# Kernel optimization log

Hardware: AMD Instinct MI355X
Metric: run time of the kernel (lower is better)

Reference implementation:

```python
import jax, jax.numpy as jnp
import numpy as np

L, B, D, H, E, K, R = 256, 64, 1024, 16, 8, 2, 64
SCALE_ADAPTER = 0.1


def setup_inputs() -> dict:
    key = jax.random.key(0)
    ks = jax.random.split(key, 10)
    rn = lambda k, shape, s=0.02: jax.random.normal(k, shape, jnp.float32) * s
    return {
        "x": jax.random.normal(ks[0], (L, B, D), jnp.float32),
        "ln1_w": jnp.ones((D,), jnp.float32), "ln1_b": jnp.zeros((D,), jnp.float32),
        "in_proj_w": rn(ks[1], (3 * D, D)), "in_proj_b": jnp.zeros((3 * D,), jnp.float32),
        "out_proj_w": rn(ks[2], (D, D)), "out_proj_b": jnp.zeros((D,), jnp.float32),
        "ln2_w": jnp.ones((D,), jnp.float32), "ln2_b": jnp.zeros((D,), jnp.float32),
        "c_fc_w": rn(ks[3], (4 * D, D)), "c_fc_b": jnp.zeros((4 * D,), jnp.float32),
        "c_proj_w": rn(ks[4], (D, 4 * D)), "c_proj_b": jnp.zeros((D,), jnp.float32),
        "w_gate": rn(ks[5], (D, E), 0.05),
        "down_w": rn(ks[6], (E, R, D)), "down_b": jnp.zeros((E, R), jnp.float32),
        "up_w": rn(ks[7], (E, D, R)), "up_b": jnp.zeros((E, D), jnp.float32),
    }


def _layer_norm(x, w, b, eps=1e-5):
    mu = x.mean(-1, keepdims=True)
    var = ((x - mu) ** 2).mean(-1, keepdims=True)
    return (x - mu) / jnp.sqrt(var + eps) * w + b


def _mha(x, in_w, in_b, out_w, out_b):
    # x: (L,B,D) sequence-first, self-attention q=k=v=x
    hd = D // H
    qkv = x @ in_w.T + in_b                       # (L,B,3D)
    q, k, v = jnp.split(qkv, 3, axis=-1)
    q = q.reshape(L, B, H, hd)
    k = k.reshape(L, B, H, hd)
    v = v.reshape(L, B, H, hd)
    scores = jnp.einsum("lbhd,mbhd->bhlm", q, k) / jnp.sqrt(jnp.float32(hd))
    attn = jax.nn.softmax(scores, axis=-1)
    o = jnp.einsum("bhlm,mbhd->lbhd", attn, v).reshape(L, B, D)
    return o @ out_w.T + out_b


def _cv_squared(t):
    t = t.astype(jnp.float32)
    return t.var(ddof=1) / (t.mean() ** 2 + 1e-10)


def reference(x, ln1_w, ln1_b, in_proj_w, in_proj_b, out_proj_w, out_proj_b,
              ln2_w, ln2_b, c_fc_w, c_fc_b, c_proj_w, c_proj_b,
              w_gate, down_w, down_b, up_w, up_b):
    x = x + _mha(_layer_norm(x, ln1_w, ln1_b), in_proj_w, in_proj_b, out_proj_w, out_proj_b)

    # --- noisy top-k gating (eval path: no noise), routed on token 0 per sequence ---
    logits = x[0] @ w_gate                                    # (B,E)
    top_v, top_i = jax.lax.top_k(logits, min(K + 1, E))
    gk = jax.nn.softmax(top_v[:, :K], axis=1)                 # (B,K)
    gates = jnp.zeros((B, E), jnp.float32).at[jnp.arange(B)[:, None], top_i[:, :K]].set(gk)
    importance = gates.sum(0)
    load = (gates > 0).sum(0)
    moe_loss = (_cv_squared(importance) + _cv_squared(load)) * 0.01

    # --- dense dispatch/combine: y[l,b] = sum_e gates[b,e] * adapter_e(x[l,b]) ---
    h = jax.nn.relu(jnp.einsum("lbd,erd->lber", x, down_w) + down_b)     # (L,B,E,R)
    y = jnp.einsum("lber,edr,be->lbd", h, up_w, gates) + (gates @ up_b)[None]
    y = y * SCALE_ADAPTER

    # --- MLP (QuickGELU) + parallel adapter residual ---
    h2 = _layer_norm(x, ln2_w, ln2_b) @ c_fc_w.T + c_fc_b
    h2 = h2 * jax.nn.sigmoid(1.702 * h2)
    mlp = h2 @ c_proj_w.T + c_proj_b
    x = x + mlp + y
    return x, moe_loss
```

## Files before the change

### kernel.cpp

```cpp
#include <hip/hip_runtime.h>

typedef unsigned short u16;
typedef unsigned int u32;
typedef __bf16 bf16x8 __attribute__((ext_vector_type(8)));
typedef float f32x4 __attribute__((ext_vector_type(4)));

#define MFMA16(a, b, c) __builtin_amdgcn_mfma_f32_16x16x32_bf16(a, b, c, 0, 0, 0)

__device__ __forceinline__ u16 f2bf(float f) {
  u32 u = __builtin_bit_cast(u32, f);
  u32 r = u + 0x7fffu + ((u >> 16) & 1u);
  return (u16)(r >> 16);
}

__device__ __forceinline__ uint4 cvt8(const float4& a, const float4& b) {
  union { u16 h[8]; uint4 q; } u;
  u.h[0] = f2bf(a.x); u.h[1] = f2bf(a.y); u.h[2] = f2bf(a.z); u.h[3] = f2bf(a.w);
  u.h[4] = f2bf(b.x); u.h[5] = f2bf(b.y); u.h[6] = f2bf(b.z); u.h[7] = f2bf(b.w);
  return u.q;
}

__device__ __forceinline__ void gload16(const u16* g, u16* l) {
  __builtin_amdgcn_global_load_lds(
      (const __attribute__((address_space(1))) u32*)g,
      (__attribute__((address_space(3))) u32*)l, 16, 0, 0);
}

template <int MODE, int ASRC>
__global__ __launch_bounds__(256) void gemm_k(
    const void* __restrict__ Av, int lda,
    const u16* __restrict__ W, int ldb,
    const float* __restrict__ bias, const float* __restrict__ aux0,
    float* __restrict__ outF, u16* __restrict__ outB, int N, int K)
{
  __shared__ u16 As[2][128 * 32];
  __shared__ u16 Bs[2][128 * 32];
  const int tid = threadIdx.x;
  const int nxb = gridDim.x >> 7;
  const int gsz = nxb << 5;
  const int g = blockIdx.x / gsz;
  const int rem = blockIdx.x - g * gsz;
  const int m0 = ((g << 5) + (rem & 31)) * 128;
  const int n0 = (rem >> 5) * 128;
  const int w = tid >> 6, lane = tid & 63, lr = lane & 15, quad = lane >> 4;
  const int wm = (w >> 1) * 64, wn = (w & 1) * 64;

  f32x4 acc[4][4];
  #pragma unroll
  for (int i = 0; i < 4; i++)
    #pragma unroll
    for (int j = 0; j < 4; j++)
      #pragma unroll
      for (int r = 0; r < 4; r++) acc[i][j][r] = 0.f;

  const int srow = w * 32 + (lane >> 2);
  const int scol = (lane & 3) * 8;
  const u16* gB0 = W + (long)(n0 + srow) * ldb + scol;
  const u16* gB1 = gB0 + (long)16 * ldb;
  const int lo = w * 1024;

  const u16* gA0 = nullptr; const u16* gA1 = nullptr;
  const float* F1 = nullptr; const float* F2 = nullptr;
  const int r0 = tid >> 2, ch0 = (tid & 3) * 8;
  if constexpr (ASRC == 0) {
    gA0 = (const u16*)Av + (long)(m0 + srow) * lda + scol;
    gA1 = gA0 + (long)16 * lda;
  } else {
    F1 = (const float*)Av + (long)(m0 + r0) * lda + ch0;
    F2 = (const float*)Av + (long)(m0 + r0 + 64) * lda + ch0;
  }

  int cur = 0;

  if constexpr (ASRC == 0) {
    gload16(gA0, &As[0][lo]);
    gload16(gA1, &As[0][lo + 512]);
    gload16(gB0, &Bs[0][lo]);
    gload16(gB1, &Bs[0][lo + 512]);
  } else {
    float4 p0 = *(const float4*)(F1);
    float4 p1 = *(const float4*)(F1 + 4);
    float4 q0 = *(const float4*)(F2);
    float4 q1 = *(const float4*)(F2 + 4);
    gload16(gB0, &Bs[0][lo]);
    gload16(gB1, &Bs[0][lo + 512]);
    *(uint4*)&As[0][r0 * 32 + ch0] = cvt8(p0, p1);
    *(uint4*)&As[0][(r0 + 64) * 32 + ch0] = cvt8(q0, q1);
  }
  __syncthreads();

  for (int k0 = 0; k0 < K; k0 += 32) {
    const int kn = k0 + 32;
    const bool more = kn < K;

    float4 p0, p1, q0, q1;
    if constexpr (ASRC == 0) {
      if (more) {
        gload16(gA0 + kn, &As[cur ^ 1][lo]);
        gload16(gA1 + kn, &As[cur ^ 1][lo + 512]);
        gload16(gB0 + kn, &Bs[cur ^ 1][lo]);
        gload16(gB1 + kn, &Bs[cur ^ 1][lo + 512]);
      }
    } else {
      if (more) {
        p0 = *(const float4*)(F1 + kn);
        p1 = *(const float4*)(F1 + kn + 4);
        q0 = *(const float4*)(F2 + kn);
        q1 = *(const float4*)(F2 + kn + 4);
        gload16(gB0 + kn, &Bs[cur ^ 1][lo]);
        gload16(gB1 + kn, &Bs[cur ^ 1][lo + 512]);
      }
    }

    const u16* Asc = As[cur];
    const u16* Bsc = Bs[cur];
    bf16x8 bfr[4];
    #pragma unroll
    for (int j = 0; j < 4; j++)
      bfr[j] = *(const bf16x8*)&Bsc[(wn + j * 16 + lr) * 32 + quad * 8];
    #pragma unroll
    for (int i = 0; i < 4; i++) {
      bf16x8 af = *(const bf16x8*)&Asc[(wm + i * 16 + lr) * 32 + quad * 8];
      #pragma unroll
      for (int j = 0; j < 4; j++)
        acc[i][j] = MFMA16(af, bfr[j], acc[i][j]);
    }

    if constexpr (ASRC == 2) {
      if (more) {
        *(uint4*)&As[cur ^ 1][r0 * 32 + ch0] = cvt8(p0, p1);
        *(uint4*)&As[cur ^ 1][(r0 + 64) * 32 + ch0] = cvt8(q0, q1);
      }
    }

    __syncthreads();
    cur ^= 1;
  }

  #pragma unroll
  for (int i = 0; i < 4; i++) {
    #pragma unroll
    for (int j = 0; j < 4; j++) {
      #pragma unroll
      for (int r = 0; r < 4; r++) {
        const int gm = m0 + wm + i * 16 + quad * 4 + r;
        const int gn = n0 + wn + j * 16 + lr;
        const long oidx = (long)gm * N + gn;
        float v = acc[i][j][r];
        if constexpr (MODE == 0) {
          v += bias[gn];
          outB[oidx] = f2bf(v);
        } else if constexpr (MODE == 1) {
          v += bias[gn] + aux0[oidx];
          outF[oidx] = v;
        } else if constexpr (MODE == 2) {
          v += bias[gn];
          v = fmaxf(v, 0.f);
          float g2 = aux0[(gm & 63) * 8 + (gn >> 6)];
          outB[oidx] = f2bf(v * g2);
        } else if constexpr (MODE == 3) {
          outF[oidx] += 0.1f * (v + aux0[(gm & 63) * 1024 + gn]);
        } else if constexpr (MODE == 4) {
          v += bias[gn];
          float e = __expf(-1.702f * v);
          v = v * __builtin_amdgcn_rcpf(1.f + e);
          outB[oidx] = f2bf(v);
        } else {
          if (bias) v += bias[gn];
          outF[oidx] += v;
        }
      }
    }
  }
}

__global__ __launch_bounds__(256) void attn_k(u16* __restrict__ qkv)
{
  __shared__ u16 Vt[64 * 264];
  __shared__ u16 Ps[32 * 264];
  __shared__ float rowstat[64];
  float* red = (float*)Ps;
  const int bh = blockIdx.x, b = bh >> 4, h = bh & 15;
  const int tid = threadIdx.x, w = tid >> 6, lane = tid & 63;
  const int lr = lane & 15, quad = lane >> 4;
  const long base = (long)b * 3072 + h * 64;

  for (int c = tid; c < 2048; c += 256) {
    int m = c >> 3, ch = (c & 7) * 8;
    uint4 vv = *(const uint4*)(qkv + (long)m * 196608 + base + 2048 + ch);
    const u16* s = (const u16*)&vv;
    #pragma unroll
    for (int t = 0; t < 8; t++) Vt[(ch + t) * 264 + m] = s[t];
  }
  __syncthreads();

  for (int qb = 0; qb < 4; qb++) {
    f32x4 acc[4][4];
    #pragma unroll
    for (int i = 0; i < 4; i++)
      #pragma unroll
      for (int j = 0; j < 4; j++)
        #pragma unroll
        for (int r = 0; r < 4; r++) acc[i][j][r] = 0.f;

    #pragma unroll
    for (int ks = 0; ks < 2; ks++) {
      bf16x8 bfr[4];
      #pragma unroll
      for (int j = 0; j < 4; j++) {
        int key = w * 64 + j * 16 + lr;
        bfr[j] = *(const bf16x8*)(qkv + (long)key * 196608 + base + 1024 + ks * 32 + quad * 8);
      }
      #pragma unroll
      for (int i = 0; i < 4; i++) {
        int gq = qb * 64 + i * 16 + lr;
        bf16x8 af = *(const bf16x8*)(qkv + (long)gq * 196608 + base + ks * 32 + quad * 8);
        #pragma unroll
        for (int j = 0; j < 4; j++)
          acc[i][j] = MFMA16(af, bfr[j], acc[i][j]);
      }
    }

    #pragma unroll
    for (int i = 0; i < 4; i++) {
      #pragma unroll
      for (int r = 0; r < 4; r++) {
        float m = -1e30f;
        #pragma unroll
        for (int j = 0; j < 4; j++) {
          float s = acc[i][j][r] * 0.125f;
          acc[i][j][r] = s;
          m = fmaxf(m, s);
        }
        #pragma unroll
        for (int off = 1; off < 16; off <<= 1) m = fmaxf(m, __shfl_xor(m, off));
        if (lr == 0) red[w * 64 + i * 16 + quad * 4 + r] = m;
      }
    }
    __syncthreads();
    if (tid < 64)
      rowstat[tid] = fmaxf(fmaxf(red[tid], red[64 + tid]),
                           fmaxf(red[128 + tid], red[192 + tid]));
    __syncthreads();

    #pragma unroll
    for (int i = 0; i < 4; i++) {
      #pragma unroll
      for (int r = 0; r < 4; r++) {
        float rm = rowstat[i * 16 + quad * 4 + r];
        float s = 0.f;
        #pragma unroll
        for (int j = 0; j < 4; j++) {
          float e = __expf(acc[i][j][r] - rm);
          acc[i][j][r] = e;
          s += e;
        }
        #pragma unroll
        for (int off = 1; off < 16; off <<= 1) s += __shfl_xor(s, off);
        if (lr == 0) red[w * 64 + i * 16 + quad * 4 + r] = s;
      }
    }
    __syncthreads();
    if (tid < 64)
      rowstat[tid] = red[tid] + red[64 + tid] + red[128 + tid] + red[192 + tid];
    __syncthreads();

    #pragma unroll
    for (int hf = 0; hf < 2; hf++) {
      #pragma unroll
      for (int ii = 0; ii < 2; ii++) {
        int i = hf * 2 + ii;
        #pragma unroll
        for (int r = 0; r < 4; r++) {
          int row = i * 16 + quad * 4 + r;
          float inv = 1.f / rowstat[row];
          #pragma unroll
          for (int j = 0; j < 4; j++)
            Ps[(row - hf * 32) * 264 + w * 64 + j * 16 + lr] =
                f2bf(acc[i][j][r] * inv);
        }
      }
      __syncthreads();
      f32x4 o[2];
      #pragma unroll
      for (int j2 = 0; j2 < 2; j2++)
        #pragma unroll
        for (int r = 0; r < 4; r++) o[j2][r] = 0.f;
      #pragma unroll
      for (int ks = 0; ks < 8; ks++) {
        bf16x8 af = *(const bf16x8*)&Ps[((w >> 1) * 16 + lr) * 264 + ks * 32 + quad * 8];
        #pragma unroll
        for (int j2 = 0; j2 < 2; j2++) {
          int j = (w & 1) * 2 + j2;
          bf16x8 bv = *(const bf16x8*)&Vt[(j * 16 + lr) * 264 + ks * 32 + quad * 8];
          o[j2] = MFMA16(af, bv, o[j2]);
        }
      }
      int l0 = qb * 64 + hf * 32 + (w >> 1) * 16 + quad * 4;
      #pragma unroll
      for (int j2 = 0; j2 < 2; j2++) {
        int j = (w & 1) * 2 + j2;
        #pragma unroll
        for (int r = 0; r < 4; r++)
          qkv[(long)(l0 + r) * 196608 + base + j * 16 + lr] = f2bf(o[j2][r]);
      }
      __syncthreads();
    }
  }
}

__global__ __launch_bounds__(256) void ln_k(const float* __restrict__ x,
                                            const float* __restrict__ wt,
                                            const float* __restrict__ bs,
                                            u16* __restrict__ out)
{
  const int tok = blockIdx.x * 4 + (threadIdx.x >> 6);
  const int lane = threadIdx.x & 63;
  const float* xp = x + (long)tok * 1024;
  float4 v[4];
  float s = 0.f, s2 = 0.f;
  #pragma unroll
  for (int t = 0; t < 4; t++) {
    v[t] = *(const float4*)(xp + t * 256 + lane * 4);
    s += v[t].x + v[t].y + v[t].z + v[t].w;
    s2 += v[t].x * v[t].x + v[t].y * v[t].y + v[t].z * v[t].z + v[t].w * v[t].w;
  }
  #pragma unroll
  for (int off = 32; off >= 1; off >>= 1) {
    s += __shfl_xor(s, off);
    s2 += __shfl_xor(s2, off);
  }
  const float m = s * (1.f / 1024.f);
  const float rstd = rsqrtf(s2 * (1.f / 1024.f) - m * m + 1e-5f);
  u16* op = out + (long)tok * 1024;
  #pragma unroll
  for (int t = 0; t < 4; t++) {
    int d = t * 256 + lane * 4;
    float4 wv = *(const float4*)(wt + d);
    float4 bv = *(const float4*)(bs + d);
    union { u16 h[4]; uint2 q; } o;
    o.h[0] = f2bf((v[t].x - m) * rstd * wv.x + bv.x);
    o.h[1] = f2bf((v[t].y - m) * rstd * wv.y + bv.y);
    o.h[2] = f2bf((v[t].z - m) * rstd * wv.z + bv.z);
    o.h[3] = f2bf((v[t].w - m) * rstd * wv.w + bv.w);
    *(uint2*)(op + d) = o.q;
  }
}

__global__ void cvtk(const float* __restrict__ src, u16* __restrict__ dst, int n4)
{
  int i = blockIdx.x * 256 + threadIdx.x;
  if (i >= n4) return;
  float4 v = ((const float4*)src)[i];
  union { u16 h[4]; uint2 q; } o;
  o.h[0] = f2bf(v.x); o.h[1] = f2bf(v.y); o.h[2] = f2bf(v.z); o.h[3] = f2bf(v.w);
  ((uint2*)dst)[i] = o.q;
}

__global__ void wupk(const float* __restrict__ up_w, u16* __restrict__ dst)
{
  int i = blockIdx.x * 256 + threadIdx.x;
  int r = i & 63, e = (i >> 6) & 7, d = i >> 9;
  dst[i] = f2bf(up_w[(e * 1024 + d) * 64 + r]);
}

__global__ __launch_bounds__(256) void gate_k(const float* __restrict__ x1,
                                              const float* __restrict__ wg,
                                              float* __restrict__ gates)
{
  const int wv = threadIdx.x >> 6, lane = threadIdx.x & 63;
  const int b = blockIdx.x * 4 + wv;
  const float* xp = x1 + (long)b * 1024;
  float lg[8];
  #pragma unroll
  for (int e = 0; e < 8; e++) lg[e] = 0.f;
  for (int i = 0; i < 16; i++) {
    int d = i * 64 + lane;
    float xv = xp[d];
    #pragma unroll
    for (int e = 0; e < 8; e++) lg[e] += xv * wg[d * 8 + e];
  }
  #pragma unroll
  for (int e = 0; e < 8; e++)
    #pragma unroll
    for (int off = 32; off >= 1; off >>= 1) lg[e] += __shfl_xor(lg[e], off);
  if (lane == 0) {
    int e1 = 0; float v1 = lg[0];
    #pragma unroll
    for (int e = 1; e < 8; e++) if (lg[e] > v1) { v1 = lg[e]; e1 = e; }
    int e2 = -1; float v2 = -1e30f;
    #pragma unroll
    for (int e = 0; e < 8; e++) if (e != e1 && lg[e] > v2) { v2 = lg[e]; e2 = e; }
    float ex = __expf(v2 - v1);
    float inv = 1.f / (1.f + ex);
    #pragma unroll
    for (int e = 0; e < 8; e++)
      gates[b * 8 + e] = (e == e1) ? inv : ((e == e2) ? ex * inv : 0.f);
  }
}

__global__ void moe_loss_k(const float* __restrict__ gates, float* __restrict__ out)
{
  if (threadIdx.x != 0) return;
  float imp[8], ld[8];
  for (int e = 0; e < 8; e++) { imp[e] = 0.f; ld[e] = 0.f; }
  for (int b = 0; b < 64; b++)
    for (int e = 0; e < 8; e++) {
      float g = gates[b * 8 + e];
      imp[e] += g;
      if (g > 0.f) ld[e] += 1.f;
    }
  float mi = 0.f, ml = 0.f;
  for (int e = 0; e < 8; e++) { mi += imp[e]; ml += ld[e]; }
  mi *= 0.125f; ml *= 0.125f;
  float vi = 0.f, vl = 0.f;
  for (int e = 0; e < 8; e++) {
    float a = imp[e] - mi; vi += a * a;
    float c = ld[e] - ml; vl += c * c;
  }
  vi *= (1.f / 7.f); vl *= (1.f / 7.f);
  out[0] = 0.01f * (vi / (mi * mi + 1e-10f) + vl / (ml * ml + 1e-10f));
}

__global__ __launch_bounds__(256) void gb_k(const float* __restrict__ gates,
                                            const float* __restrict__ up_b,
                                            float* __restrict__ gb)
{
  int b = blockIdx.x, d0 = threadIdx.x * 4;
  float g[8];
  #pragma unroll
  for (int e = 0; e < 8; e++) g[e] = gates[b * 8 + e];
  float s0 = 0, s1 = 0, s2 = 0, s3 = 0;
  #pragma unroll
  for (int e = 0; e < 8; e++) {
    float4 u = *(const float4*)(up_b + e * 1024 + d0);
    s0 += g[e] * u.x; s1 += g[e] * u.y; s2 += g[e] * u.z; s3 += g[e] * u.w;
  }
  float4 r; r.x = s0; r.y = s1; r.z = s2; r.w = s3;
  *(float4*)(gb + b * 1024 + d0) = r;
}

extern "C" void kernel_launch(void* const* d_in, const int* in_sizes, int n_in,
                              void* d_out, int out_size, void* d_ws, size_t ws_size,
                              hipStream_t stream)
{
  (void)in_sizes; (void)n_in; (void)out_size;
  const float* x      = (const float*)d_in[0];
  const float* ln1_w  = (const float*)d_in[1];
  const float* ln1_b  = (const float*)d_in[2];
  const float* in_w   = (const float*)d_in[3];
  const float* in_b   = (const float*)d_in[4];
  const float* out_w  = (const float*)d_in[5];
  const float* out_b  = (const float*)d_in[6];
  const float* ln2_w  = (const float*)d_in[7];
  const float* ln2_b  = (const float*)d_in[8];
  const float* fc_w   = (const float*)d_in[9];
  const float* fc_b   = (const float*)d_in[10];
  const float* pj_w   = (const float*)d_in[11];
  const float* pj_b   = (const float*)d_in[12];
  const float* w_gate = (const float*)d_in[13];
  const float* down_w = (const float*)d_in[14];
  const float* down_b = (const float*)d_in[15];
  const float* up_w   = (const float*)d_in[16];
  const float* up_b   = (const float*)d_in[17];
  float* out = (float*)d_out;
  char* ws = (char*)d_ws;

  u16* wb_in   = (u16*)(ws + 0);
  u16* wb_out  = (u16*)(ws + 6291456);
  u16* wb_down = (u16*)(ws + 8388608);
  u16* wb_up   = (u16*)(ws + 9437184);
  u16* wb_fc   = (u16*)(ws + 0);
  u16* wb_pj   = (u16*)(ws + 10485760);
  float* gates = (float*)(ws + 19005440);
  float* gb    = (float*)(ws + 19007488);
  u16* qkv     = (u16*)(ws + 19269632);
  u16* xln2    = (u16*)(ws + 19269632);
  u16* hg      = (u16*)(ws + 52824064);
  u16* h2      = (u16*)(ws + 69601280);
  u16* xln = (u16*)d_out;

  const bool big = ws_size >= (size_t)203819008;

  cvtk<<<3072, 256, 0, stream>>>(in_w, wb_in, 786432);
  cvtk<<<1024, 256, 0, stream>>>(out_w, wb_out, 262144);
  cvtk<<<512, 256, 0, stream>>>(down_w, wb_down, 131072);
  wupk<<<2048, 256, 0, stream>>>(up_w, wb_up);

  ln_k<<<4096, 256, 0, stream>>>(x, ln1_w, ln1_b, xln);
  gemm_k<0, 0><<<24 * 128, 256, 0, stream>>>(
      xln, 1024, wb_in, 1024, in_b, nullptr, nullptr, qkv, 3072, 1024);

  attn_k<<<1024, 256, 0, stream>>>(qkv);

  gemm_k<1, 0><<<8 * 128, 256, 0, stream>>>(
      qkv, 3072, wb_out, 1024, out_b, x, out, nullptr, 1024, 1024);

  gate_k<<<16, 256, 0, stream>>>(out, w_gate, gates);
  moe_loss_k<<<1, 64, 0, stream>>>(gates, out + 16777216);
  gb_k<<<64, 256, 0, stream>>>(gates, up_b, gb);

  ln_k<<<4096, 256, 0, stream>>>(out, ln2_w, ln2_b, xln2);

  gemm_k<2, 2><<<4 * 128, 256, 0, stream>>>(
      out, 1024, wb_down, 1024, down_b, gates, nullptr, hg, 512, 1024);
  gemm_k<3, 0><<<8 * 128, 256, 0, stream>>>(
      hg, 512, wb_up, 512, nullptr, gb, out, nullptr, 1024, 512);

  cvtk<<<4096, 256, 0, stream>>>(fc_w, wb_fc, 1048576);
  cvtk<<<4096, 256, 0, stream>>>(pj_w, wb_pj, 1048576);

  if (big) {
    gemm_k<4, 0><<<32 * 128, 256, 0, stream>>>(
        xln2, 1024, wb_fc, 1024, fc_b, nullptr, nullptr, h2, 4096, 1024);
    gemm_k<5, 0><<<8 * 128, 256, 0, stream>>>(
        h2, 4096, wb_pj, 4096, pj_b, nullptr, out, nullptr, 1024, 4096);
  } else {
    for (int c = 0; c < 4; c++) {
      gemm_k<4, 0><<<8 * 128, 256, 0, stream>>>(
          xln2, 1024, wb_fc + (long)c * 1048576, 1024, fc_b + c * 1024,
          nullptr, nullptr, h2, 1024, 1024);
      gemm_k<5, 0><<<8 * 128, 256, 0, stream>>>(
          h2, 1024, wb_pj + c * 1024, 4096, (c == 0) ? pj_b : nullptr,
          nullptr, out, nullptr, 1024, 1024);
    }
  }
}
```

Measured before the change: 1.053 ms.

## Deepen GEMM async LDS pipeline to four stages with vmcnt waits

For bf16-input GEMMs the shared-memory ring grows from two to four buffers. Three tiles are prefetched with direct global-to-LDS loads, and explicit s_waitcnt vmcnt counts replace the full sync, so only one barrier per k-step remains. The goal is to hide global memory latency better. In exchange it uses twice the LDS, which may lower occupancy, and the hand-written waitcnt assumes every thread issues exactly four loads per stage.

```diff
diff --git a/kernel.cpp b/kernel.cpp
--- a/kernel.cpp
+++ b/kernel.cpp
@@ -33,8 +33,9 @@
     const float* __restrict__ bias, const float* __restrict__ aux0,
     float* __restrict__ outF, u16* __restrict__ outB, int N, int K)
 {
-  __shared__ u16 As[2][128 * 32];
-  __shared__ u16 Bs[2][128 * 32];
+  constexpr int NBUF = (ASRC == 0) ? 4 : 2;
+  __shared__ u16 As[NBUF][128 * 32];
+  __shared__ u16 Bs[NBUF][128 * 32];
   const int tid = threadIdx.x;
   const int nxb = gridDim.x >> 7;
   const int gsz = nxb << 5;
@@ -70,38 +71,65 @@
     F2 = (const float*)Av + (long)(m0 + r0 + 64) * lda + ch0;
   }
 
-  int cur = 0;
+  auto compute_tile = [&](const u16* Asc, const u16* Bsc) {
+    bf16x8 bfr[4];
+    #pragma unroll
+    for (int j = 0; j < 4; j++)
+      bfr[j] = *(const bf16x8*)&Bsc[(wn + j * 16 + lr) * 32 + quad * 8];
+    #pragma unroll
+    for (int i = 0; i < 4; i++) {
+      bf16x8 af = *(const bf16x8*)&Asc[(wm + i * 16 + lr) * 32 + quad * 8];
+      #pragma unroll
+      for (int j = 0; j < 4; j++)
+        acc[i][j] = MFMA16(af, bfr[j], acc[i][j]);
+    }
+  };
 
   if constexpr (ASRC == 0) {
-    gload16(gA0, &As[0][lo]);
-    gload16(gA1, &As[0][lo + 512]);
-    gload16(gB0, &Bs[0][lo]);
-    gload16(gB1, &Bs[0][lo + 512]);
+    const int nt = K >> 5;
+    #pragma unroll
+    for (int p = 0; p < 3; p++) {
+      const int kk = p * 32;
+      gload16(gA0 + kk, &As[p][lo]);
+      gload16(gA1 + kk, &As[p][lo + 512]);
+      gload16(gB0 + kk, &Bs[p][lo]);
+      gload16(gB1 + kk, &Bs[p][lo + 512]);
+    }
+    for (int t = 0; t < nt; t++) {
+      if (t < nt - 2)      asm volatile("s_waitcnt vmcnt(8)" ::: "memory");
+      else if (t < nt - 1) asm volatile("s_waitcnt vmcnt(4)" ::: "memory");
+      else                 asm volatile("s_waitcnt vmcnt(0)" ::: "memory");
+      __builtin_amdgcn_s_barrier();
+      asm volatile("" ::: "memory");
+      const int tp = t + 3;
+      if (tp < nt) {
+        const int kn = tp * 32;
+        u16* a = As[tp & 3];
+        u16* b = Bs[tp & 3];
+        gload16(gA0 + kn, a + lo);
+        gload16(gA1 + kn, a + lo + 512);
+        gload16(gB0 + kn, b + lo);
+        gload16(gB1 + kn, b + lo + 512);
+      }
+      compute_tile(As[t & 3], Bs[t & 3]);
+    }
   } else {
-    float4 p0 = *(const float4*)(F1);
-    float4 p1 = *(const float4*)(F1 + 4);
-    float4 q0 = *(const float4*)(F2);
-    float4 q1 = *(const float4*)(F2 + 4);
-    gload16(gB0, &Bs[0][lo]);
-    gload16(gB1, &Bs[0][lo + 512]);
-    *(uint4*)&As[0][r0 * 32 + ch0] = cvt8(p0, p1);
-    *(uint4*)&As[0][(r0 + 64) * 32 + ch0] = cvt8(q0, q1);
-  }
-  __syncthreads();
-
-  for (int k0 = 0; k0 < K; k0 += 32) {
-    const int kn = k0 + 32;
-    const bool more = kn < K;
-
-    float4 p0, p1, q0, q1;
-    if constexpr (ASRC == 0) {
-      if (more) {
-        gload16(gA0 + kn, &As[cur ^ 1][lo]);
-        gload16(gA1 + kn, &As[cur ^ 1][lo + 512]);
-        gload16(gB0 + kn, &Bs[cur ^ 1][lo]);
-        gload16(gB1 + kn, &Bs[cur ^ 1][lo + 512]);
-      }
-    } else {
+    int cur = 0;
+    {
+      float4 p0 = *(const float4*)(F1);
+      float4 p1 = *(const float4*)(F1 + 4);
+      float4 q0 = *(const float4*)(F2);
+      float4 q1 = *(const float4*)(F2 + 4);
+      gload16(gB0, &Bs[0][lo]);
+      gload16(gB1, &Bs[0][lo + 512]);
+      *(uint4*)&As[0][r0 * 32 + ch0] = cvt8(p0, p1);
+      *(uint4*)&As[0][(r0 + 64) * 32 + ch0] = cvt8(q0, q1);
+    }
+    __syncthreads();
+    for (int k0 = 0; k0 < K; k0 += 32) {
+      const int kn = k0 + 32;
+      const bool more = kn < K;
+      float4 p0, p1, q0, q1;
       if (more) {
         p0 = *(const float4*)(F1 + kn);
         p1 = *(const float4*)(F1 + kn + 4);
@@ -110,31 +138,14 @@
         gload16(gB0 + kn, &Bs[cur ^ 1][lo]);
         gload16(gB1 + kn, &Bs[cur ^ 1][lo + 512]);
       }
-    }
-
-    const u16* Asc = As[cur];
-    const u16* Bsc = Bs[cur];
-    bf16x8 bfr[4];
-    #pragma unroll
-    for (int j = 0; j < 4; j++)
-      bfr[j] = *(const bf16x8*)&Bsc[(wn + j * 16 + lr) * 32 + quad * 8];
-    #pragma unroll
-    for (int i = 0; i < 4; i++) {
-      bf16x8 af = *(const bf16x8*)&Asc[(wm + i * 16 + lr) * 32 + quad * 8];
-      #pragma unroll
-      for (int j = 0; j < 4; j++)
-        acc[i][j] = MFMA16(af, bfr[j], acc[i][j]);
-    }
-
-    if constexpr (ASRC == 2) {
+      compute_tile(As[cur], Bs[cur]);
       if (more) {
         *(uint4*)&As[cur ^ 1][r0 * 32 + ch0] = cvt8(p0, p1);
         *(uint4*)&As[cur ^ 1][(r0 + 64) * 32 + ch0] = cvt8(q0, q1);
       }
-    }
-
-    __syncthreads();
-    cur ^= 1;
+      __syncthreads();
+      cur ^= 1;
+    }
   }
 
   #pragma unroll
```

Result: slower. 1.109 ms (+5.3%).
